# Kernel tuning notes

Hardware: AMD Instinct MI355X
Metric: run time of the kernel (lower is better)

The kernel has to match this reference:

```python
import jax, jax.numpy as jnp
import numpy as np

H, D = 16, 64  # num_heads, head_dim (d_model = 1024)


def setup_inputs() -> dict:
    key = jax.random.key(0)
    ks = jax.random.split(key, 5)
    B, S, E = 2, 2048, H * D
    scale = 0.02  # keep logits in a sane range
    return {
        "x": jax.random.normal(ks[0], (B, S, E), jnp.float32),
        "Wq": jax.random.normal(ks[1], (E, E), jnp.float32) * scale,
        "bq": jnp.zeros((E,), jnp.float32),
        "Wk": jax.random.normal(ks[2], (E, E), jnp.float32) * scale,
        "bk": jnp.zeros((E,), jnp.float32),
        "Wv": jax.random.normal(ks[3], (E, E), jnp.float32) * scale,
        "bv": jnp.zeros((E,), jnp.float32),
        "Wo": jax.random.normal(ks[4], (E, E), jnp.float32) * scale,
        "bo": jnp.zeros((E,), jnp.float32),
    }


def reference(x, Wq, bq, Wk, bk, Wv, bv, Wo, bo):
    B, S, E = x.shape

    def proj(W, b):
        # torch nn.Linear: x @ W.T + b; then split heads -> [B, H, S, D]
        return (x @ W.T + b).reshape(B, S, H, D).transpose(0, 2, 1, 3)

    q = proj(Wq, bq)
    k = proj(Wk, bk)
    v = proj(Wv, bv)

    # scores [B, H, S, S]; original masks with -inf BEFORE scaling (-inf/scale == -inf)
    att = jnp.einsum("bhqd,bhkd->bhqk", q, k)
    causal = jnp.triu(jnp.ones((S, S), bool), k=1)  # True above diagonal
    att = jnp.where(causal, -jnp.inf, att) * jnp.float32(1.0 / np.sqrt(D))
    att = jax.nn.softmax(att, axis=-1)

    ctx = jnp.einsum("bhqk,bhkd->bhqd", att, v)  # [B, H, S, D]
    ctx = ctx.transpose(0, 2, 1, 3).reshape(B, S, H * D)  # merge heads
    return ctx @ Wo.T + bo
```

## Files before the change

### kernel.cpp

```cpp
#include <hip/hip_runtime.h>
#include <hip/hip_bf16.h>

#define S_LEN 2048
#define NH    16
#define HD    64
#define EMB   1024
#define BATCH 2
#define M_TOT 4096

typedef __attribute__((ext_vector_type(8)))  __bf16   bf16x8;
typedef __attribute__((ext_vector_type(4)))  __bf16   bf16x4;
typedef __attribute__((ext_vector_type(4)))  float    f32x4;
typedef __attribute__((ext_vector_type(16))) float    f32x16;
typedef __attribute__((ext_vector_type(4)))  unsigned u32x4;

static __device__ __forceinline__ unsigned pk2(float a, float b) {
    unsigned short ua = __builtin_bit_cast(unsigned short, (__bf16)a);
    unsigned short ub = __builtin_bit_cast(unsigned short, (__bf16)b);
    return (unsigned)ua | ((unsigned)ub << 16);
}

__global__ __launch_bounds__(256) void cast_all(const float* __restrict__ x,
        const float* __restrict__ wq, const float* __restrict__ wk,
        const float* __restrict__ wv, const float* __restrict__ wo,
        __bf16* __restrict__ xb, __bf16* __restrict__ wqb,
        __bf16* __restrict__ wkb, __bf16* __restrict__ wvb,
        __bf16* __restrict__ wob) {
    int i = blockIdx.x * 256 + threadIdx.x;
    const float* src; __bf16* dst; int j;
    if (i < (1 << 20)) { src = x; dst = xb; j = i; }
    else {
        int t = i - (1 << 20);
        int r = t >> 18;
        j = t & ((1 << 18) - 1);
        src = (r == 0) ? wq : (r == 1) ? wk : (r == 2) ? wv : wo;
        dst = (r == 0) ? wqb : (r == 1) ? wkb : (r == 2) ? wvb : wob;
    }
    f32x4 v = ((const f32x4*)src)[j];
    bf16x4 o;
    o[0] = (__bf16)v[0]; o[1] = (__bf16)v[1];
    o[2] = (__bf16)v[2]; o[3] = (__bf16)v[3];
    ((bf16x4*)dst)[j] = o;
}

__global__ __launch_bounds__(256) void gemm_qkv(const __bf16* __restrict__ A,
        const __bf16* __restrict__ Wq, const __bf16* __restrict__ Wk,
        const __bf16* __restrict__ Wv,
        const float* __restrict__ bq, const float* __restrict__ bk,
        const float* __restrict__ bv,
        __bf16* __restrict__ Qo, __bf16* __restrict__ Ko, __bf16* __restrict__ Vo) {
    __shared__ __bf16 As[128][64];
    __shared__ __bf16 Bs[128][64];

    const int z = blockIdx.z;
    const __bf16* Bw   = (z == 0) ? Wq : (z == 1) ? Wk : Wv;
    const float*  bias = (z == 0) ? bq : (z == 1) ? bk : bv;
    __bf16*       outp = (z == 0) ? Qo : (z == 1) ? Ko : Vo;

    const int tid  = threadIdx.x;
    const int wid  = tid >> 6;
    const int lane = tid & 63;
    const int lrow = lane & 15;
    const int lhi  = lane >> 4;
    const int m0 = blockIdx.y * 128;
    const int n0 = blockIdx.x * 128;
    const int wr = wid >> 1, wc = wid & 1;

    const int lr8 = lane >> 3;
    const int lc8 = (lane & 7) * 8;

    f32x4 acc[4][4];
#pragma unroll
    for (int i = 0; i < 4; ++i)
#pragma unroll
        for (int j = 0; j < 4; ++j)
            acc[i][j] = (f32x4){0.f, 0.f, 0.f, 0.f};

    for (int k0 = 0; k0 < EMB; k0 += 64) {
#pragma unroll
        for (int t = 0; t < 4; ++t) {
            const int row = wid * 32 + t * 8;
            __builtin_amdgcn_global_load_lds(
                (const __attribute__((address_space(1))) void*)&A[(size_t)(m0 + row + lr8) * EMB + k0 + lc8],
                (__attribute__((address_space(3))) void*)&As[row][0], 16, 0, 0);
            __builtin_amdgcn_global_load_lds(
                (const __attribute__((address_space(1))) void*)&Bw[(size_t)(n0 + row + lr8) * EMB + k0 + lc8],
                (__attribute__((address_space(3))) void*)&Bs[row][0], 16, 0, 0);
        }
        __syncthreads();
#pragma unroll
        for (int kk = 0; kk < 2; ++kk) {
            bf16x8 af[4], bfr[4];
#pragma unroll
            for (int i = 0; i < 4; ++i)
                af[i] = *(const bf16x8*)&As[wr * 64 + i * 16 + lrow][kk * 32 + lhi * 8];
#pragma unroll
            for (int j = 0; j < 4; ++j)
                bfr[j] = *(const bf16x8*)&Bs[wc * 64 + j * 16 + lrow][kk * 32 + lhi * 8];
#pragma unroll
            for (int i = 0; i < 4; ++i)
#pragma unroll
                for (int j = 0; j < 4; ++j)
                    acc[i][j] = __builtin_amdgcn_mfma_f32_16x16x32_bf16(af[i], bfr[j], acc[i][j], 0, 0, 0);
        }
        __syncthreads();
    }

#pragma unroll
    for (int i = 0; i < 4; ++i) {
#pragma unroll
        for (int j = 0; j < 4; ++j) {
#pragma unroll
            for (int jj = 0; jj < 4; ++jj) {
                int row = m0 + wr * 64 + i * 16 + lhi * 4 + jj;
                int col = n0 + wc * 64 + j * 16 + lrow;
                float v = acc[i][j][jj] + bias[col];
                int b = row >> 11, s = row & (S_LEN - 1);
                int h = col >> 6,  d = col & (HD - 1);
                size_t idx = (z == 2)
                    ? ((size_t)(b * NH + h) * HD + d) * S_LEN + s
                    : ((size_t)(b * NH + h) * S_LEN + s) * HD + d;
                outp[idx] = (__bf16)v;
            }
        }
    }
}

__global__ __launch_bounds__(256) void gemm_out(const __bf16* __restrict__ A,
        const __bf16* __restrict__ Bw, const float* __restrict__ bias,
        float* __restrict__ outp) {
    __shared__ __bf16 As[128][64];
    __shared__ __bf16 Bs[128][64];

    const int tid  = threadIdx.x;
    const int wid  = tid >> 6;
    const int lane = tid & 63;
    const int lrow = lane & 15;
    const int lhi  = lane >> 4;
    const int m0 = blockIdx.y * 128;
    const int n0 = blockIdx.x * 128;
    const int wr = wid >> 1, wc = wid & 1;
    const int lr8 = lane >> 3;
    const int lc8 = (lane & 7) * 8;

    f32x4 acc[4][4];
#pragma unroll
    for (int i = 0; i < 4; ++i)
#pragma unroll
        for (int j = 0; j < 4; ++j)
            acc[i][j] = (f32x4){0.f, 0.f, 0.f, 0.f};

    for (int k0 = 0; k0 < EMB; k0 += 64) {
#pragma unroll
        for (int t = 0; t < 4; ++t) {
            const int row = wid * 32 + t * 8;
            __builtin_amdgcn_global_load_lds(
                (const __attribute__((address_space(1))) void*)&A[(size_t)(m0 + row + lr8) * EMB + k0 + lc8],
                (__attribute__((address_space(3))) void*)&As[row][0], 16, 0, 0);
            __builtin_amdgcn_global_load_lds(
                (const __attribute__((address_space(1))) void*)&Bw[(size_t)(n0 + row + lr8) * EMB + k0 + lc8],
                (__attribute__((address_space(3))) void*)&Bs[row][0], 16, 0, 0);
        }
        __syncthreads();
#pragma unroll
        for (int kk = 0; kk < 2; ++kk) {
            bf16x8 af[4], bfr[4];
#pragma unroll
            for (int i = 0; i < 4; ++i)
                af[i] = *(const bf16x8*)&As[wr * 64 + i * 16 + lrow][kk * 32 + lhi * 8];
#pragma unroll
            for (int j = 0; j < 4; ++j)
                bfr[j] = *(const bf16x8*)&Bs[wc * 64 + j * 16 + lrow][kk * 32 + lhi * 8];
#pragma unroll
            for (int i = 0; i < 4; ++i)
#pragma unroll
                for (int j = 0; j < 4; ++j)
                    acc[i][j] = __builtin_amdgcn_mfma_f32_16x16x32_bf16(af[i], bfr[j], acc[i][j], 0, 0, 0);
        }
        __syncthreads();
    }

#pragma unroll
    for (int i = 0; i < 4; ++i)
#pragma unroll
        for (int j = 0; j < 4; ++j)
#pragma unroll
            for (int jj = 0; jj < 4; ++jj) {
                int row = m0 + wr * 64 + i * 16 + lhi * 4 + jj;
                int col = n0 + wc * 64 + j * 16 + lrow;
                outp[(size_t)row * EMB + col] = acc[i][j][jj] + bias[col];
            }
}

__global__ __launch_bounds__(256) void attn_kernel(const __bf16* __restrict__ Q,
        const __bf16* __restrict__ K, const __bf16* __restrict__ Vt,
        __bf16* __restrict__ ctx) {
    __shared__ float Of[4][32][65];
    __shared__ float MLs[4][2][32];

    const int wid  = threadIdx.x >> 6;
    const int lane = threadIdx.x & 63;
    const int lq   = lane & 31;
    const int hi   = lane >> 5;
    const int bid  = blockIdx.x;
    const int xcd  = bid & 7;
    const int idx  = bid >> 3;
    const int qt   = 63 - (idx & 63);
    const int bh   = xcd + 8 * (idx >> 6);
    const int q0   = qt * 32;

    const __bf16* Qh = Q  + (size_t)bh * S_LEN * HD;
    const __bf16* Kh = K  + (size_t)bh * S_LEN * HD;
    const __bf16* Vh = Vt + (size_t)bh * HD * S_LEN;

    bf16x8 qf[4];
#pragma unroll
    for (int ds = 0; ds < 4; ++ds) {
        bf16x8 t = *(const bf16x8*)&Qh[(size_t)(q0 + lq) * HD + ds * 16 + hi * 8];
#pragma unroll
        for (int j = 0; j < 8; ++j) qf[ds][j] = (__bf16)((float)t[j] * 0.125f);
    }

    f32x16 o0, o1;
#pragma unroll
    for (int r = 0; r < 16; ++r) { o0[r] = 0.f; o1[r] = 0.f; }
    float m = -1e30f, l = 0.f;

    const int nkt = qt + 1;

    bf16x8 kf0, kf1, kf2, kf3;
    if (wid < nkt) {
        const __bf16* kp = &Kh[(size_t)(wid * 32 + lq) * HD + hi * 8];
        kf0 = *(const bf16x8*)(kp);      kf1 = *(const bf16x8*)(kp + 16);
        kf2 = *(const bf16x8*)(kp + 32); kf3 = *(const bf16x8*)(kp + 48);
    }

    for (int kt = wid; kt < nkt; kt += 4) {
        const int kk0 = kt * 32;

        bf16x8 va0 = *(const bf16x8*)&Vh[(size_t)lq * S_LEN + kk0 + hi * 8];
        bf16x8 vb0 = *(const bf16x8*)&Vh[(size_t)lq * S_LEN + kk0 + 16 + hi * 8];
        bf16x8 va1 = *(const bf16x8*)&Vh[(size_t)(32 + lq) * S_LEN + kk0 + hi * 8];
        bf16x8 vb1 = *(const bf16x8*)&Vh[(size_t)(32 + lq) * S_LEN + kk0 + 16 + hi * 8];

        const int nk0 = (kt + 4 < nkt ? kt + 4 : kt) * 32;
        bf16x8 nkf0, nkf1, nkf2, nkf3;
        {
            const __bf16* kp = &Kh[(size_t)(nk0 + lq) * HD + hi * 8];
            nkf0 = *(const bf16x8*)(kp);      nkf1 = *(const bf16x8*)(kp + 16);
            nkf2 = *(const bf16x8*)(kp + 32); nkf3 = *(const bf16x8*)(kp + 48);
        }

        f32x16 s;
#pragma unroll
        for (int r = 0; r < 16; ++r) s[r] = 0.f;
        s = __builtin_amdgcn_mfma_f32_32x32x16_bf16(kf0, qf[0], s, 0, 0, 0);
        s = __builtin_amdgcn_mfma_f32_32x32x16_bf16(kf1, qf[1], s, 0, 0, 0);
        s = __builtin_amdgcn_mfma_f32_32x32x16_bf16(kf2, qf[2], s, 0, 0, 0);
        s = __builtin_amdgcn_mfma_f32_32x32x16_bf16(kf3, qf[3], s, 0, 0, 0);

        if (kk0 == q0) {
#pragma unroll
            for (int r = 0; r < 16; ++r) {
                int keyl = (r & 3) + 8 * (r >> 2) + 4 * hi;
                s[r] = (keyl <= lq) ? s[r] : -1e30f;
            }
        }

        float pm = s[0];
#pragma unroll
        for (int r = 1; r < 16; ++r) pm = fmaxf(pm, s[r]);
        pm = fmaxf(pm, __shfl_xor(pm, 32));

        float mn = fmaxf(m, pm);
        float f  = __expf(m - mn);
        m = mn;

        float ps = 0.f;
#pragma unroll
        for (int r = 0; r < 16; ++r) { s[r] = __expf(s[r] - mn); ps += s[r]; }
        ps += __shfl_xor(ps, 32);
        l = l * f + ps;

#pragma unroll
        for (int r = 0; r < 16; ++r) { o0[r] *= f; o1[r] *= f; }

        unsigned w0 = pk2(s[0],  s[1]),  w1 = pk2(s[2],  s[3]);
        unsigned w2 = pk2(s[4],  s[5]),  w3 = pk2(s[6],  s[7]);
        unsigned w4 = pk2(s[8],  s[9]),  w5 = pk2(s[10], s[11]);
        unsigned w6 = pk2(s[12], s[13]), w7 = pk2(s[14], s[15]);

        unsigned e0 = (unsigned)__shfl_xor((int)(hi ? w0 : w2), 32);
        unsigned e1 = (unsigned)__shfl_xor((int)(hi ? w1 : w3), 32);
        unsigned e2 = (unsigned)__shfl_xor((int)(hi ? w4 : w6), 32);
        unsigned e3 = (unsigned)__shfl_xor((int)(hi ? w5 : w7), 32);
        u32x4 pb0, pb1;
        if (hi) { pb0 = (u32x4){e0, e1, w2, w3}; pb1 = (u32x4){e2, e3, w6, w7}; }
        else    { pb0 = (u32x4){w0, w1, e0, e1}; pb1 = (u32x4){w4, w5, e2, e3}; }
        bf16x8 pb0b = __builtin_bit_cast(bf16x8, pb0);
        bf16x8 pb1b = __builtin_bit_cast(bf16x8, pb1);

        o0 = __builtin_amdgcn_mfma_f32_32x32x16_bf16(va0, pb0b, o0, 0, 0, 0);
        o0 = __builtin_amdgcn_mfma_f32_32x32x16_bf16(vb0, pb1b, o0, 0, 0, 0);
        o1 = __builtin_amdgcn_mfma_f32_32x32x16_bf16(va1, pb0b, o1, 0, 0, 0);
        o1 = __builtin_amdgcn_mfma_f32_32x32x16_bf16(vb1, pb1b, o1, 0, 0, 0);

        kf0 = nkf0; kf1 = nkf1; kf2 = nkf2; kf3 = nkf3;
    }

#pragma unroll
    for (int r = 0; r < 16; ++r) {
        int d0 = (r & 3) + 8 * (r >> 2) + 4 * hi;
        Of[wid][lq][d0]      = o0[r];
        Of[wid][lq][32 + d0] = o1[r];
    }
    if (lane < 32) { MLs[wid][0][lq] = m; MLs[wid][1][lq] = l; }
    __syncthreads();

    {
        const int tq = threadIdx.x >> 3;
        const int d8 = (threadIdx.x & 7) * 8;
        float m0_ = MLs[0][0][tq], m1_ = MLs[1][0][tq];
        float m2_ = MLs[2][0][tq], m3_ = MLs[3][0][tq];
        float M = fmaxf(fmaxf(m0_, m1_), fmaxf(m2_, m3_));
        float a0 = __expf(m0_ - M), a1 = __expf(m1_ - M);
        float a2 = __expf(m2_ - M), a3 = __expf(m3_ - M);
        float L = MLs[0][1][tq] * a0 + MLs[1][1][tq] * a1
                + MLs[2][1][tq] * a2 + MLs[3][1][tq] * a3;
        float invL = 1.f / L;
        const int b = bh >> 4, h = bh & 15;
        bf16x8 outv;
#pragma unroll
        for (int e = 0; e < 8; ++e) {
            int d = d8 + e;
            float v = a0 * Of[0][tq][d] + a1 * Of[1][tq][d]
                    + a2 * Of[2][tq][d] + a3 * Of[3][tq][d];
            outv[e] = (__bf16)(v * invL);
        }
        *(bf16x8*)&ctx[((size_t)b * S_LEN + q0 + tq) * EMB + h * HD + d8] = outv;
    }
}

extern "C" void kernel_launch(void* const* d_in, const int* in_sizes, int n_in,
                              void* d_out, int out_size, void* d_ws, size_t ws_size,
                              hipStream_t stream) {
    const float* x  = (const float*)d_in[0];
    const float* Wq = (const float*)d_in[1];
    const float* bq = (const float*)d_in[2];
    const float* Wk = (const float*)d_in[3];
    const float* bk = (const float*)d_in[4];
    const float* Wv = (const float*)d_in[5];
    const float* bv = (const float*)d_in[6];
    const float* Wo = (const float*)d_in[7];
    const float* bo = (const float*)d_in[8];

    char* ws = (char*)d_ws;
    __bf16* xb  = (__bf16*)(ws);
    __bf16* Wqb = (__bf16*)(ws + ( 8ull << 20));
    __bf16* Wkb = (__bf16*)(ws + (10ull << 20));
    __bf16* Wvb = (__bf16*)(ws + (12ull << 20));
    __bf16* Wob = (__bf16*)(ws + (14ull << 20));
    __bf16* Qb  = (__bf16*)(ws + (16ull << 20));
    __bf16* Kb  = (__bf16*)(ws + (24ull << 20));
    __bf16* Vtb = (__bf16*)(ws + (32ull << 20));
    __bf16* Cb  = (__bf16*)(ws + (40ull << 20));

    cast_all<<<8192, 256, 0, stream>>>(x, Wq, Wk, Wv, Wo, xb, Wqb, Wkb, Wvb, Wob);

    gemm_qkv<<<dim3(EMB / 128, M_TOT / 128, 3), 256, 0, stream>>>(
        xb, Wqb, Wkb, Wvb, bq, bk, bv, Qb, Kb, Vtb);

    attn_kernel<<<dim3(2048), 256, 0, stream>>>(Qb, Kb, Vtb, Cb);

    gemm_out<<<dim3(EMB / 128, M_TOT / 128), 256, 0, stream>>>(Cb, Wob, bo, (float*)d_out);
}
```

Baseline: 257.4 us.

## Double-buffer GEMM LDS tiles and add lazy softmax rescaling in attention

Measured after the change: 238.8 us. 7.3% less time.

```diff
diff --git a/kernel.cpp b/kernel.cpp
--- a/kernel.cpp
+++ b/kernel.cpp
@@ -43,14 +43,43 @@
     ((bf16x4*)dst)[j] = o;
 }
 
+#define GEMM_STAGE(Abuf, Bbuf, Asrc, Bsrc, k0)                                            \
+    _Pragma("unroll")                                                                     \
+    for (int t = 0; t < 4; ++t) {                                                         \
+        const int row = wid * 32 + t * 8;                                                 \
+        __builtin_amdgcn_global_load_lds(                                                 \
+            (const __attribute__((address_space(1))) void*)&Asrc[(size_t)(m0 + row + lr8) * EMB + (k0) + lc8], \
+            (__attribute__((address_space(3))) void*)&Abuf[row][0], 16, 0, 0);            \
+        __builtin_amdgcn_global_load_lds(                                                 \
+            (const __attribute__((address_space(1))) void*)&Bsrc[(size_t)(n0 + row + lr8) * EMB + (k0) + lc8], \
+            (__attribute__((address_space(3))) void*)&Bbuf[row][0], 16, 0, 0);            \
+    }
+
+#define GEMM_COMPUTE(Abuf, Bbuf)                                                          \
+    _Pragma("unroll")                                                                     \
+    for (int kk = 0; kk < 2; ++kk) {                                                      \
+        bf16x8 af[4], bfr[4];                                                             \
+        _Pragma("unroll")                                                                 \
+        for (int i = 0; i < 4; ++i)                                                       \
+            af[i] = *(const bf16x8*)&Abuf[wr * 64 + i * 16 + lrow][kk * 32 + lhi * 8];    \
+        _Pragma("unroll")                                                                 \
+        for (int j = 0; j < 4; ++j)                                                       \
+            bfr[j] = *(const bf16x8*)&Bbuf[wc * 64 + j * 16 + lrow][kk * 32 + lhi * 8];   \
+        _Pragma("unroll")                                                                 \
+        for (int i = 0; i < 4; ++i)                                                       \
+            _Pragma("unroll")                                                             \
+            for (int j = 0; j < 4; ++j)                                                   \
+                acc[i][j] = __builtin_amdgcn_mfma_f32_16x16x32_bf16(af[i], bfr[j], acc[i][j], 0, 0, 0); \
+    }
+
 __global__ __launch_bounds__(256) void gemm_qkv(const __bf16* __restrict__ A,
         const __bf16* __restrict__ Wq, const __bf16* __restrict__ Wk,
         const __bf16* __restrict__ Wv,
         const float* __restrict__ bq, const float* __restrict__ bk,
         const float* __restrict__ bv,
         __bf16* __restrict__ Qo, __bf16* __restrict__ Ko, __bf16* __restrict__ Vo) {
-    __shared__ __bf16 As[128][64];
-    __shared__ __bf16 Bs[128][64];
+    __shared__ __bf16 As0[128][64], As1[128][64];
+    __shared__ __bf16 Bs0[128][64], Bs1[128][64];
 
     const int z = blockIdx.z;
     const __bf16* Bw   = (z == 0) ? Wq : (z == 1) ? Wk : Wv;
@@ -65,7 +94,6 @@
     const int m0 = blockIdx.y * 128;
     const int n0 = blockIdx.x * 128;
     const int wr = wid >> 1, wc = wid & 1;
-
     const int lr8 = lane >> 3;
     const int lc8 = (lane & 7) * 8;
 
@@ -76,33 +104,14 @@
         for (int j = 0; j < 4; ++j)
             acc[i][j] = (f32x4){0.f, 0.f, 0.f, 0.f};
 
-    for (int k0 = 0; k0 < EMB; k0 += 64) {
-#pragma unroll
-        for (int t = 0; t < 4; ++t) {
-            const int row = wid * 32 + t * 8;
-            __builtin_amdgcn_global_load_lds(
-                (const __attribute__((address_space(1))) void*)&A[(size_t)(m0 + row + lr8) * EMB + k0 + lc8],
-                (__attribute__((address_space(3))) void*)&As[row][0], 16, 0, 0);
-            __builtin_amdgcn_global_load_lds(
-                (const __attribute__((address_space(1))) void*)&Bw[(size_t)(n0 + row + lr8) * EMB + k0 + lc8],
-                (__attribute__((address_space(3))) void*)&Bs[row][0], 16, 0, 0);
-        }
+    GEMM_STAGE(As0, Bs0, A, Bw, 0)
+    __syncthreads();
+    for (int kt = 0; kt < 16; kt += 2) {
+        GEMM_STAGE(As1, Bs1, A, Bw, (kt + 1) * 64)
+        GEMM_COMPUTE(As0, Bs0)
         __syncthreads();
-#pragma unroll
-        for (int kk = 0; kk < 2; ++kk) {
-            bf16x8 af[4], bfr[4];
-#pragma unroll
-            for (int i = 0; i < 4; ++i)
-                af[i] = *(const bf16x8*)&As[wr * 64 + i * 16 + lrow][kk * 32 + lhi * 8];
-#pragma unroll
-            for (int j = 0; j < 4; ++j)
-                bfr[j] = *(const bf16x8*)&Bs[wc * 64 + j * 16 + lrow][kk * 32 + lhi * 8];
-#pragma unroll
-            for (int i = 0; i < 4; ++i)
-#pragma unroll
-                for (int j = 0; j < 4; ++j)
-                    acc[i][j] = __builtin_amdgcn_mfma_f32_16x16x32_bf16(af[i], bfr[j], acc[i][j], 0, 0, 0);
-        }
+        if (kt + 2 < 16) { GEMM_STAGE(As0, Bs0, A, Bw, (kt + 2) * 64) }
+        GEMM_COMPUTE(As1, Bs1)
         __syncthreads();
     }
 
@@ -129,8 +138,8 @@
 __global__ __launch_bounds__(256) void gemm_out(const __bf16* __restrict__ A,
         const __bf16* __restrict__ Bw, const float* __restrict__ bias,
         float* __restrict__ outp) {
-    __shared__ __bf16 As[128][64];
-    __shared__ __bf16 Bs[128][64];
+    __shared__ __bf16 As0[128][64], As1[128][64];
+    __shared__ __bf16 Bs0[128][64], Bs1[128][64];
 
     const int tid  = threadIdx.x;
     const int wid  = tid >> 6;
@@ -150,33 +159,14 @@
         for (int j = 0; j < 4; ++j)
             acc[i][j] = (f32x4){0.f, 0.f, 0.f, 0.f};
 
-    for (int k0 = 0; k0 < EMB; k0 += 64) {
-#pragma unroll
-        for (int t = 0; t < 4; ++t) {
-            const int row = wid * 32 + t * 8;
-            __builtin_amdgcn_global_load_lds(
-                (const __attribute__((address_space(1))) void*)&A[(size_t)(m0 + row + lr8) * EMB + k0 + lc8],
-                (__attribute__((address_space(3))) void*)&As[row][0], 16, 0, 0);
-            __builtin_amdgcn_global_load_lds(
-                (const __attribute__((address_space(1))) void*)&Bw[(size_t)(n0 + row + lr8) * EMB + k0 + lc8],
-                (__attribute__((address_space(3))) void*)&Bs[row][0], 16, 0, 0);
-        }
+    GEMM_STAGE(As0, Bs0, A, Bw, 0)
+    __syncthreads();
+    for (int kt = 0; kt < 16; kt += 2) {
+        GEMM_STAGE(As1, Bs1, A, Bw, (kt + 1) * 64)
+        GEMM_COMPUTE(As0, Bs0)
         __syncthreads();
-#pragma unroll
-        for (int kk = 0; kk < 2; ++kk) {
-            bf16x8 af[4], bfr[4];
-#pragma unroll
-            for (int i = 0; i < 4; ++i)
-                af[i] = *(const bf16x8*)&As[wr * 64 + i * 16 + lrow][kk * 32 + lhi * 8];
-#pragma unroll
-            for (int j = 0; j < 4; ++j)
-                bfr[j] = *(const bf16x8*)&Bs[wc * 64 + j * 16 + lrow][kk * 32 + lhi * 8];
-#pragma unroll
-            for (int i = 0; i < 4; ++i)
-#pragma unroll
-                for (int j = 0; j < 4; ++j)
-                    acc[i][j] = __builtin_amdgcn_mfma_f32_16x16x32_bf16(af[i], bfr[j], acc[i][j], 0, 0, 0);
-        }
+        if (kt + 2 < 16) { GEMM_STAGE(As0, Bs0, A, Bw, (kt + 2) * 64) }
+        GEMM_COMPUTE(As1, Bs1)
         __syncthreads();
     }
 
@@ -272,18 +262,20 @@
         for (int r = 1; r < 16; ++r) pm = fmaxf(pm, s[r]);
         pm = fmaxf(pm, __shfl_xor(pm, 32));
 
-        float mn = fmaxf(m, pm);
-        float f  = __expf(m - mn);
-        m = mn;
+        if (!__all(pm - m <= 8.f)) {
+            float mn = fmaxf(m, pm);
+            float f  = __expf(m - mn);
+            l *= f;
+#pragma unroll
+            for (int r = 0; r < 16; ++r) { o0[r] *= f; o1[r] *= f; }
+            m = mn;
+        }
 
         float ps = 0.f;
 #pragma unroll
-        for (int r = 0; r < 16; ++r) { s[r] = __expf(s[r] - mn); ps += s[r]; }
+        for (int r = 0; r < 16; ++r) { s[r] = __expf(s[r] - m); ps += s[r]; }
         ps += __shfl_xor(ps, 32);
-        l = l * f + ps;
-
-#pragma unroll
-        for (int r = 0; r < 16; ++r) { o0[r] *= f; o1[r] *= f; }
+        l += ps;
 
         unsigned w0 = pk2(s[0],  s[1]),  w1 = pk2(s[2],  s[3]);
         unsigned w2 = pk2(s[4],  s[5]),  w3 = pk2(s[6],  s[7]);
@@ -295,8 +287,10 @@
         unsigned e2 = (unsigned)__shfl_xor((int)(hi ? w4 : w6), 32);
         unsigned e3 = (unsigned)__shfl_xor((int)(hi ? w5 : w7), 32);
         u32x4 pb0, pb1;
-        if (hi) { pb0 = (u32x4){e0, e1, w2, w3}; pb1 = (u32x4){e2, e3, w6, w7}; }
-        else    { pb0 = (u32x4){w0, w1, e0, e1}; pb1 = (u32x4){w4, w5, e2, e3}; }
+        pb0[0] = hi ? e0 : w0;  pb0[1] = hi ? e1 : w1;
+        pb0[2] = hi ? w2 : e0;  pb0[3] = hi ? w3 : e1;
+        pb1[0] = hi ? e2 : w4;  pb1[1] = hi ? e3 : w5;
+        pb1[2] = hi ? w6 : e2;  pb1[3] = hi ? w7 : e3;
         bf16x8 pb0b = __builtin_bit_cast(bf16x8, pb0);
         bf16x8 pb1b = __builtin_bit_cast(bf16x8, pb1);
 
```
